# Performance work log

Hardware: AMD Instinct MI355X
Metric: run time of the kernel (lower is better)

Reference implementation:

```python
import jax, jax.numpy as jnp
import numpy as np

N_NODES = 50000
N_EDGES = 800000
IN_DIM = 512
HEADS = 4
HID = 64
OUT = 64
NEG_SLOPE = 0.2  # DGL GATConv default


def gat_layer(x, W, attn_l, attn_r, bias, src, dst, n_nodes, heads, d_out):
    # x: [N, F_in], W: [F_in, heads*d_out], attn_l/attn_r: [heads, d_out], bias: [heads, d_out]
    f = (x @ W).reshape(n_nodes, heads, d_out)          # [N, H, D]
    el = jnp.sum(f * attn_l, axis=-1)                   # [N, H]
    er = jnp.sum(f * attn_r, axis=-1)                   # [N, H]
    e = jax.nn.leaky_relu(el[src] + er[dst], NEG_SLOPE) # [E, H]
    # segment softmax over incoming edges of each dst node
    m = jax.ops.segment_max(e, dst, num_segments=n_nodes)       # [N, H]
    ex = jnp.exp(e - m[dst])                                     # [E, H]
    den = jax.ops.segment_sum(ex, dst, num_segments=n_nodes)    # [N, H]
    a = ex / den[dst]                                            # [E, H]
    # scatter-aggregate weighted messages
    out = jax.ops.segment_sum(a[:, :, None] * f[src], dst, num_segments=n_nodes)  # [N, H, D]
    return out + bias, a


def setup_inputs() -> dict:
    key = jax.random.key(0)
    ks = jax.random.split(key, 12)
    features = jax.random.normal(ks[0], (N_NODES, IN_DIM), dtype=jnp.float32)
    src = jax.random.randint(ks[1], (N_EDGES,), 0, N_NODES, dtype=jnp.int32)
    dst = jax.random.randint(ks[2], (N_EDGES,), 0, N_NODES, dtype=jnp.int32)
    s1 = 1.0 / np.sqrt(IN_DIM)
    s2 = 1.0 / np.sqrt(HEADS * HID)
    W1 = jax.random.normal(ks[3], (IN_DIM, HEADS * HID), dtype=jnp.float32) * s1
    al1 = jax.random.normal(ks[4], (HEADS, HID), dtype=jnp.float32) * s1
    ar1 = jax.random.normal(ks[5], (HEADS, HID), dtype=jnp.float32) * s1
    b1 = jnp.zeros((HEADS, HID), dtype=jnp.float32)
    W2 = jax.random.normal(ks[6], (HEADS * HID, OUT), dtype=jnp.float32) * s2
    al2 = jax.random.normal(ks[7], (1, OUT), dtype=jnp.float32) * s2
    ar2 = jax.random.normal(ks[8], (1, OUT), dtype=jnp.float32) * s2
    b2 = jnp.zeros((1, OUT), dtype=jnp.float32)
    return {"features": features, "W1": W1, "al1": al1, "ar1": ar1, "b1": b1,
            "W2": W2, "al2": al2, "ar2": ar2, "b2": b2, "src": src, "dst": dst}


def reference(features, W1, al1, ar1, b1, W2, al2, ar2, b2, src, dst):
    h1, _ = gat_layer(features, W1, al1, ar1, b1, src, dst, N_NODES, HEADS, HID)
    h1 = jax.nn.elu(h1.reshape(N_NODES, HEADS * HID))   # flatten heads + ELU
    h2, _ = gat_layer(h1, W2, al2, ar2, b2, src, dst, N_NODES, 1, OUT)
    return h2  # [N, 1, OUT]
```

## Files before the change

### kernel.cpp

```cpp
#include <hip/hip_runtime.h>

#define N_NODES 50000
#define N_EDGES 800000
#define IN_DIM 512
#define NEG_SLOPE 0.2f

typedef short short8 __attribute__((ext_vector_type(8)));
typedef float f32x16 __attribute__((ext_vector_type(16)));
typedef __attribute__((address_space(3))) unsigned int lds_u32;
typedef const __attribute__((address_space(1))) unsigned int glb_u32;

__device__ __forceinline__ unsigned bf16rne(float f) {
  union { float f; unsigned u; } v;
  v.f = f;
  return (v.u + 0x7FFFu + ((v.u >> 16) & 1u)) >> 16;
}
__device__ __forceinline__ void tsplit8(float4 a, float4 b, short8& hi,
                                        short8& lo) {
  float fa[8] = {a.x, a.y, a.z, a.w, b.x, b.y, b.z, b.w};
#pragma unroll
  for (int i = 0; i < 8; i++) {
    unsigned u = __float_as_uint(fa[i]);
    hi[i] = (short)(u >> 16);
    float lof = fa[i] - __uint_as_float(u & 0xffff0000u);
    lo[i] = (short)(__float_as_uint(lof) >> 16);
  }
}

__global__ void pack_w(const float* __restrict__ W, short* __restrict__ Bhi,
                       int N) {
  int k = blockIdx.x, n = threadIdx.x;
  float w = W[(size_t)k * N + n];
  int ksub = k >> 4, kh = (k >> 3) & 1, j = k & 7;
  int nsub = n >> 5, lane2 = (n & 31) | (kh << 5);
  size_t off = (((size_t)ksub * (N >> 5) + nsub) * 64 + lane2) * 8 + j;
  Bhi[off] = (short)bf16rne(w);
}

template <int K, int NSUBS, int NTILES>
__global__ __launch_bounds__(256) void gemm_mfma(
    const float* __restrict__ A, const short* __restrict__ Bhi_,
    unsigned short* __restrict__ Cb, const float* __restrict__ alv,
    const float* __restrict__ arv, float* __restrict__ el,
    float* __restrict__ er, int M) {
  constexpr int N = NSUBS * 32;
  constexpr int MT = 4 / NTILES;
  constexpr int BROWS = MT * 32;
  constexpr int T = K / 32;
  __shared__ float ldsb[2][BROWS * 32];

  const int tid = threadIdx.x;
  const int lane = tid & 63;
  const int w = tid >> 6;
  const int l31 = lane & 31;
  const int half = lane >> 5;
  const int local_mt = w / NTILES;
  const int ntile = w % NTILES;
  const int block_row0 = blockIdx.x * BROWS;

  const float* gsrc[MT];
#pragma unroll
  for (int q = 0; q < MT; q++) {
    int seg = w * MT + q;
    int r = seg * 8 + (lane >> 3);
    int c = (lane & 7) ^ (r & 7);
    int grow = block_row0 + r;
    if (grow > M - 1) grow = M - 1;
    gsrc[q] = A + (size_t)grow * K + c * 4;
  }
  unsigned lbase[MT];
#pragma unroll
  for (int q = 0; q < MT; q++) lbase[q] = (w * MT + q) * 256;

  const short8* bh = (const short8*)Bhi_;
  const size_t bbase = (size_t)(ntile * 2) * 64 + lane;

  const int arow = local_mt * 32 + l31;
  const int rs = arow & 7;

  f32x16 acc0 = {}, acc1 = {};
  short8 cb0[2], cb1[2];

#pragma unroll
  for (int q = 0; q < MT; q++) {
    __builtin_amdgcn_global_load_lds((glb_u32*)(gsrc[q]),
                                     (lds_u32*)&ldsb[0][lbase[q]], 16, 0, 0);
  }
#pragma unroll
  for (int u = 0; u < 2; u++) {
    size_t bb = bbase + (size_t)u * NSUBS * 64;
    cb0[u] = bh[bb];
    cb1[u] = bh[bb + 64];
  }
  __syncthreads();

  int buf = 0;
  for (int t = 0; t < T; t++) {
    if (t + 1 < T) {
      int kb = (t + 1) * 32;
#pragma unroll
      for (int q = 0; q < MT; q++) {
        __builtin_amdgcn_global_load_lds((glb_u32*)(gsrc[q] + kb),
                                         (lds_u32*)&ldsb[buf ^ 1][lbase[q]],
                                         16, 0, 0);
      }
    }
    int tn = (t + 1 < T) ? t + 1 : t;
    short8 nb0[2], nb1[2];
#pragma unroll
    for (int u = 0; u < 2; u++) {
      size_t bb = bbase + (size_t)(tn * 2 + u) * NSUBS * 64;
      nb0[u] = bh[bb];
      nb1[u] = bh[bb + 64];
    }
    const float* lb = ldsb[buf];
#pragma unroll
    for (int u = 0; u < 2; u++) {
      int c0 = u * 4 + half * 2;
      float4 a0 = *(const float4*)&lb[arow * 32 + (c0 ^ rs) * 4];
      float4 a1 = *(const float4*)&lb[arow * 32 + ((c0 + 1) ^ rs) * 4];
      short8 ah, al8;
      tsplit8(a0, a1, ah, al8);
      acc0 = __builtin_amdgcn_mfma_f32_32x32x16_bf16(ah, cb0[u], acc0, 0, 0, 0);
      acc0 = __builtin_amdgcn_mfma_f32_32x32x16_bf16(al8, cb0[u], acc0, 0, 0, 0);
      acc1 = __builtin_amdgcn_mfma_f32_32x32x16_bf16(ah, cb1[u], acc1, 0, 0, 0);
      acc1 = __builtin_amdgcn_mfma_f32_32x32x16_bf16(al8, cb1[u], acc1, 0, 0, 0);
    }
    __syncthreads();
#pragma unroll
    for (int u = 0; u < 2; u++) {
      cb0[u] = nb0[u];
      cb1[u] = nb1[u];
    }
    buf ^= 1;
  }

  int colbase = ntile * 64 + l31;
  float wa0 = alv[colbase], wa1 = alv[colbase + 32];
  float wr0 = arv[colbase], wr1 = arv[colbase + 32];
  const int mrow0 = block_row0 + local_mt * 32;
#pragma unroll
  for (int r = 0; r < 16; r++) {
    int roff = (r & 3) + 8 * (r >> 2) + 4 * half;
    int row = mrow0 + roff;
    if (row < M) {
      Cb[(size_t)row * N + colbase] = (unsigned short)bf16rne(acc0[r]);
      Cb[(size_t)row * N + colbase + 32] = (unsigned short)bf16rne(acc1[r]);
    }
    float elv = acc0[r] * wa0 + acc1[r] * wa1;
    float erv = acc0[r] * wr0 + acc1[r] * wr1;
#pragma unroll
    for (int off = 1; off < 32; off <<= 1) {
      elv += __shfl_xor(elv, off);
      erv += __shfl_xor(erv, off);
    }
    if (l31 == 0 && row < M) {
      el[row * NTILES + ntile] = elv;
      er[row * NTILES + ntile] = erv;
    }
  }
}

__global__ void hist_kernel(const int* __restrict__ dst,
                            int* __restrict__ counts) {
  int e = blockIdx.x * blockDim.x + threadIdx.x;
  if (e < N_EDGES) atomicAdd(&counts[dst[e]], 1);
}

#define NSCAN 196
__global__ __launch_bounds__(256) void scan_part(const int* __restrict__ counts,
                                                 int* __restrict__ offsets,
                                                 int* __restrict__ bsums) {
  __shared__ int sh[256];
  int t = threadIdx.x;
  int i = blockIdx.x * 256 + t;
  int v = (i < N_NODES) ? counts[i] : 0;
  sh[t] = v;
  __syncthreads();
  for (int o = 1; o < 256; o <<= 1) {
    int x = (t >= o) ? sh[t - o] : 0;
    __syncthreads();
    sh[t] += x;
    __syncthreads();
  }
  if (i < N_NODES) offsets[i] = sh[t] - v;
  if (t == 255) bsums[blockIdx.x] = sh[255];
}
__global__ __launch_bounds__(256) void scan_top(int* __restrict__ bsums) {
  __shared__ int sh[256];
  int t = threadIdx.x;
  int v = (t < NSCAN) ? bsums[t] : 0;
  sh[t] = v;
  __syncthreads();
  for (int o = 1; o < 256; o <<= 1) {
    int x = (t >= o) ? sh[t - o] : 0;
    __syncthreads();
    sh[t] += x;
    __syncthreads();
  }
  if (t < NSCAN) bsums[t] = sh[t] - v;
}
__global__ __launch_bounds__(256) void scan_add(int* __restrict__ offsets,
                                                const int* __restrict__ bsums) {
  int i = blockIdx.x * 256 + threadIdx.x;
  if (i < N_NODES) offsets[i] += bsums[blockIdx.x];
  if (i == 0) offsets[N_NODES] = N_EDGES;
}

__global__ void scatter_kernel(const int* __restrict__ src,
                               const int* __restrict__ dst,
                               const int* __restrict__ offsets,
                               int* __restrict__ fill,
                               int* __restrict__ csr_src) {
  int e = blockIdx.x * blockDim.x + threadIdx.x;
  if (e < N_EDGES) {
    int d = dst[e];
    int pos = offsets[d] + atomicAdd(&fill[d], 1);
    csr_src[pos] = src[e];
  }
}

__global__ __launch_bounds__(256) void agg1_kernel(
    const int* __restrict__ offsets, const int* __restrict__ csr_src,
    const float* __restrict__ el, const float* __restrict__ er,
    const unsigned short* __restrict__ fb, const float* __restrict__ bias,
    float* __restrict__ h1) {
  __shared__ float red[3][256];
  __shared__ float dred[3][32];
  int n = blockIdx.x;
  int t = threadIdx.x;
  int w = t >> 6, lane = t & 63;
  int l31 = lane & 31;
  int eslot = lane >> 5;
  int h = l31 >> 3;
  int slot = w * 2 + eslot;
  int off0 = offsets[n], deg = offsets[n + 1] - off0;
  float erh = er[n * 4 + h];
  float4 aLo = {0.f, 0.f, 0.f, 0.f}, aHi = {0.f, 0.f, 0.f, 0.f};
  float4 bLo = {0.f, 0.f, 0.f, 0.f}, bHi = {0.f, 0.f, 0.f, 0.f};
  float sden = 0.f;
  int i = slot;
  for (; i + 8 < deg; i += 16) {
    int s0 = csr_src[off0 + i];
    int s1 = csr_src[off0 + i + 8];
    uint4 p0 = *(const uint4*)(fb + (size_t)s0 * 256 + l31 * 8);
    uint4 p1 = *(const uint4*)(fb + (size_t)s1 * 256 + l31 * 8);
    float e0 = el[s0 * 4 + h] + erh;
    float e1 = el[s1 * 4 + h] + erh;
    e0 = e0 > 0.f ? e0 : NEG_SLOPE * e0;
    e1 = e1 > 0.f ? e1 : NEG_SLOPE * e1;
    float a0 = __expf(e0), a1 = __expf(e1);
    sden += a0 + a1;
    aLo.x += a0 * __uint_as_float(p0.x << 16);
    aLo.y += a0 * __uint_as_float(p0.x & 0xffff0000u);
    aLo.z += a0 * __uint_as_float(p0.y << 16);
    aLo.w += a0 * __uint_as_float(p0.y & 0xffff0000u);
    aHi.x += a0 * __uint_as_float(p0.z << 16);
    aHi.y += a0 * __uint_as_float(p0.z & 0xffff0000u);
    aHi.z += a0 * __uint_as_float(p0.w << 16);
    aHi.w += a0 * __uint_as_float(p0.w & 0xffff0000u);
    bLo.x += a1 * __uint_as_float(p1.x << 16);
    bLo.y += a1 * __uint_as_float(p1.x & 0xffff0000u);
    bLo.z += a1 * __uint_as_float(p1.y << 16);
    bLo.w += a1 * __uint_as_float(p1.y & 0xffff0000u);
    bHi.x += a1 * __uint_as_float(p1.z << 16);
    bHi.y += a1 * __uint_as_float(p1.z & 0xffff0000u);
    bHi.z += a1 * __uint_as_float(p1.w << 16);
    bHi.w += a1 * __uint_as_float(p1.w & 0xffff0000u);
  }
  if (i < deg) {
    int s0 = csr_src[off0 + i];
    uint4 p0 = *(const uint4*)(fb + (size_t)s0 * 256 + l31 * 8);
    float e0 = el[s0 * 4 + h] + erh;
    e0 = e0 > 0.f ? e0 : NEG_SLOPE * e0;
    float a0 = __expf(e0);
    sden += a0;
    aLo.x += a0 * __uint_as_float(p0.x << 16);
    aLo.y += a0 * __uint_as_float(p0.x & 0xffff0000u);
    aLo.z += a0 * __uint_as_float(p0.y << 16);
    aLo.w += a0 * __uint_as_float(p0.y & 0xffff0000u);
    aHi.x += a0 * __uint_as_float(p0.z << 16);
    aHi.y += a0 * __uint_as_float(p0.z & 0xffff0000u);
    aHi.z += a0 * __uint_as_float(p0.w << 16);
    aHi.w += a0 * __uint_as_float(p0.w & 0xffff0000u);
  }
  aLo.x += bLo.x; aLo.y += bLo.y; aLo.z += bLo.z; aLo.w += bLo.w;
  aHi.x += bHi.x; aHi.y += bHi.y; aHi.z += bHi.z; aHi.w += bHi.w;
  aLo.x += __shfl_xor(aLo.x, 32);
  aLo.y += __shfl_xor(aLo.y, 32);
  aLo.z += __shfl_xor(aLo.z, 32);
  aLo.w += __shfl_xor(aLo.w, 32);
  aHi.x += __shfl_xor(aHi.x, 32);
  aHi.y += __shfl_xor(aHi.y, 32);
  aHi.z += __shfl_xor(aHi.z, 32);
  aHi.w += __shfl_xor(aHi.w, 32);
  sden += __shfl_xor(sden, 32);
  if (w && lane < 32) {
    *(float4*)(&red[w - 1][l31 * 8]) = aLo;
    *(float4*)(&red[w - 1][l31 * 8 + 4]) = aHi;
    dred[w - 1][l31] = sden;
  }
  __syncthreads();
  if (w == 0 && lane < 32) {
    float den = sden;
#pragma unroll
    for (int j = 0; j < 3; j++) {
      float4 rL = *(float4*)(&red[j][l31 * 8]);
      float4 rH = *(float4*)(&red[j][l31 * 8 + 4]);
      aLo.x += rL.x; aLo.y += rL.y; aLo.z += rL.z; aLo.w += rL.w;
      aHi.x += rH.x; aHi.y += rH.y; aHi.z += rH.z; aHi.w += rH.w;
      den += dred[j][l31];
    }
    float invd = den > 0.f ? 1.0f / den : 0.f;
    float4 b0 = ((const float4*)bias)[l31 * 2];
    float4 b1 = ((const float4*)bias)[l31 * 2 + 1];
    float o[8] = {aLo.x * invd + b0.x, aLo.y * invd + b0.y,
                  aLo.z * invd + b0.z, aLo.w * invd + b0.w,
                  aHi.x * invd + b1.x, aHi.y * invd + b1.y,
                  aHi.z * invd + b1.z, aHi.w * invd + b1.w};
#pragma unroll
    for (int j = 0; j < 8; j++) o[j] = o[j] > 0.f ? o[j] : __expf(o[j]) - 1.0f;
    float4 o0 = {o[0], o[1], o[2], o[3]};
    float4 o1 = {o[4], o[5], o[6], o[7]};
    *(float4*)(h1 + (size_t)n * 256 + l31 * 8) = o0;
    *(float4*)(h1 + (size_t)n * 256 + l31 * 8 + 4) = o1;
  }
}

__global__ __launch_bounds__(256) void agg2_kernel(
    const int* __restrict__ offsets, const int* __restrict__ csr_src,
    const float* __restrict__ el, const float* __restrict__ er,
    const unsigned short* __restrict__ fb2, const float* __restrict__ bias,
    float* __restrict__ out) {
  int w = threadIdx.x >> 6, lane = threadIdx.x & 63;
  int n = blockIdx.x * 4 + w;
  if (n >= N_NODES) return;
  int dg = lane & 15, eslot = lane >> 4;
  int off0 = offsets[n], deg = offsets[n + 1] - off0;
  float ern = er[n];
  float4 acc = {0.f, 0.f, 0.f, 0.f};
  float4 acc2 = {0.f, 0.f, 0.f, 0.f};
  float sden = 0.f;
  int i = eslot;
  for (; i + 4 < deg; i += 8) {
    int s0 = csr_src[off0 + i];
    int s1 = csr_src[off0 + i + 4];
    uint2 p0 = *(const uint2*)(fb2 + (size_t)s0 * 64 + dg * 4);
    uint2 p1 = *(const uint2*)(fb2 + (size_t)s1 * 64 + dg * 4);
    float e0 = el[s0] + ern;
    float e1 = el[s1] + ern;
    e0 = e0 > 0.f ? e0 : NEG_SLOPE * e0;
    e1 = e1 > 0.f ? e1 : NEG_SLOPE * e1;
    float a0 = __expf(e0), a1 = __expf(e1);
    sden += a0 + a1;
    acc.x += a0 * __uint_as_float(p0.x << 16);
    acc.y += a0 * __uint_as_float(p0.x & 0xffff0000u);
    acc.z += a0 * __uint_as_float(p0.y << 16);
    acc.w += a0 * __uint_as_float(p0.y & 0xffff0000u);
    acc2.x += a1 * __uint_as_float(p1.x << 16);
    acc2.y += a1 * __uint_as_float(p1.x & 0xffff0000u);
    acc2.z += a1 * __uint_as_float(p1.y << 16);
    acc2.w += a1 * __uint_as_float(p1.y & 0xffff0000u);
  }
  if (i < deg) {
    int s0 = csr_src[off0 + i];
    uint2 p0 = *(const uint2*)(fb2 + (size_t)s0 * 64 + dg * 4);
    float e0 = el[s0] + ern;
    e0 = e0 > 0.f ? e0 : NEG_SLOPE * e0;
    float a0 = __expf(e0);
    sden += a0;
    acc.x += a0 * __uint_as_float(p0.x << 16);
    acc.y += a0 * __uint_as_float(p0.x & 0xffff0000u);
    acc.z += a0 * __uint_as_float(p0.y << 16);
    acc.w += a0 * __uint_as_float(p0.y & 0xffff0000u);
  }
  acc.x += acc2.x;
  acc.y += acc2.y;
  acc.z += acc2.z;
  acc.w += acc2.w;
#pragma unroll
  for (int off = 16; off < 64; off <<= 1) {
    acc.x += __shfl_xor(acc.x, off);
    acc.y += __shfl_xor(acc.y, off);
    acc.z += __shfl_xor(acc.z, off);
    acc.w += __shfl_xor(acc.w, off);
    sden += __shfl_xor(sden, off);
  }
  if (eslot == 0) {
    float invd = sden > 0.f ? 1.0f / sden : 0.f;
    float4 b = ((const float4*)bias)[dg];
    float4 ov = {acc.x * invd + b.x, acc.y * invd + b.y, acc.z * invd + b.z,
                 acc.w * invd + b.w};
    *(float4*)(out + (size_t)n * 64 + dg * 4) = ov;
  }
}

extern "C" void kernel_launch(void* const* d_in, const int* in_sizes, int n_in,
                              void* d_out, int out_size, void* d_ws,
                              size_t ws_size, hipStream_t stream) {
  const float* features = (const float*)d_in[0];
  const float* W1 = (const float*)d_in[1];
  const float* al1 = (const float*)d_in[2];
  const float* ar1 = (const float*)d_in[3];
  const float* b1 = (const float*)d_in[4];
  const float* W2 = (const float*)d_in[5];
  const float* al2 = (const float*)d_in[6];
  const float* ar2 = (const float*)d_in[7];
  const float* b2 = (const float*)d_in[8];
  const int* src = (const int*)d_in[9];
  const int* dst = (const int*)d_in[10];
  float* out = (float*)d_out;

  float* h1 = (float*)d_ws;
  unsigned short* fb = (unsigned short*)(h1 + (size_t)N_NODES * 256);
  unsigned short* fb2 = fb;
  float* el1 = (float*)(fb + (size_t)N_NODES * 256);
  float* er1 = el1 + N_NODES * 4;
  float* el2 = er1 + N_NODES * 4;
  float* er2 = el2 + N_NODES;
  int* counts = (int*)(er2 + N_NODES);
  int* offsets = counts + N_NODES;
  int* fill = offsets + N_NODES + 1;
  int* csr_src = fill + N_NODES;
  int* bsums = csr_src + N_EDGES;

  short* b1hi = (short*)d_out;
  short* b2hi = (short*)fill;

  hipMemsetAsync(counts, 0, N_NODES * sizeof(int), stream);
  hipMemsetAsync(fill, 0, N_NODES * sizeof(int), stream);
  hist_kernel<<<(N_EDGES + 255) / 256, 256, 0, stream>>>(dst, counts);
  scan_part<<<NSCAN, 256, 0, stream>>>(counts, offsets, bsums);
  scan_top<<<1, 256, 0, stream>>>(bsums);
  scan_add<<<NSCAN, 256, 0, stream>>>(offsets, bsums);
  scatter_kernel<<<(N_EDGES + 255) / 256, 256, 0, stream>>>(src, dst, offsets,
                                                            fill, csr_src);

  pack_w<<<512, 256, 0, stream>>>(W1, b1hi, 256);
  pack_w<<<256, 64, 0, stream>>>(W2, b2hi, 64);

  gemm_mfma<IN_DIM, 8, 4><<<1563, 256, 0, stream>>>(features, b1hi, fb, al1,
                                                    ar1, el1, er1, N_NODES);
  agg1_kernel<<<N_NODES, 256, 0, stream>>>(offsets, csr_src, el1, er1, fb, b1,
                                           h1);

  gemm_mfma<256, 2, 1><<<391, 256, 0, stream>>>(h1, b2hi, fb2, al2, ar2, el2,
                                                er2, N_NODES);
  agg2_kernel<<<(N_NODES + 3) / 4, 256, 0, stream>>>(offsets, csr_src, el2,
                                                     er2, fb2, b2, out);
}
```

Measured before the change: 408.2 us.

## Deepen GEMM K-step to 64 and add row-group register blocking

The MFMA GEMM now stages 64-wide K slices per iteration instead of 32, halving the number of barrier-separated steps, and adds an RG template parameter so each wave computes multiple 32-row groups, reusing loaded B fragments across them. Layer 1 uses RG=2, which halves the grid, and launch bounds request two blocks per CU. This is meant to cut per-step sync overhead and B-fragment loads, in exchange for more LDS and register use, which may lower occupancy.

```diff
diff --git a/kernel.cpp b/kernel.cpp
--- a/kernel.cpp
+++ b/kernel.cpp
@@ -37,17 +37,18 @@
   Bhi[off] = (short)bf16rne(w);
 }
 
-template <int K, int NSUBS, int NTILES>
-__global__ __launch_bounds__(256) void gemm_mfma(
+template <int K, int NSUBS, int NTILES, int RG>
+__global__ __launch_bounds__(256, 2) void gemm_mfma(
     const float* __restrict__ A, const short* __restrict__ Bhi_,
     unsigned short* __restrict__ Cb, const float* __restrict__ alv,
     const float* __restrict__ arv, float* __restrict__ el,
     float* __restrict__ er, int M) {
   constexpr int N = NSUBS * 32;
   constexpr int MT = 4 / NTILES;
-  constexpr int BROWS = MT * 32;
-  constexpr int T = K / 32;
-  __shared__ float ldsb[2][BROWS * 32];
+  constexpr int BROWS = MT * RG * 32;
+  constexpr int T = K / 64;
+  constexpr int GPW = BROWS / 16;
+  __shared__ float ldsb[2][BROWS * 64];
 
   const int tid = threadIdx.x;
   const int lane = tid & 63;
@@ -58,79 +59,89 @@
   const int ntile = w % NTILES;
   const int block_row0 = blockIdx.x * BROWS;
 
-  const float* gsrc[MT];
-#pragma unroll
-  for (int q = 0; q < MT; q++) {
-    int seg = w * MT + q;
-    int r = seg * 8 + (lane >> 3);
-    int c = (lane & 7) ^ (r & 7);
+  const float* gsrc[GPW];
+#pragma unroll
+  for (int q = 0; q < GPW; q++) {
+    int g = w * GPW + q;
+    int r = g * 4 + (lane >> 4);
+    int p = lane & 15;
+    int c = (p & 8) | ((p & 7) ^ (r & 7));
     int grow = block_row0 + r;
     if (grow > M - 1) grow = M - 1;
     gsrc[q] = A + (size_t)grow * K + c * 4;
   }
-  unsigned lbase[MT];
-#pragma unroll
-  for (int q = 0; q < MT; q++) lbase[q] = (w * MT + q) * 256;
 
   const short8* bh = (const short8*)Bhi_;
-  const size_t bbase = (size_t)(ntile * 2) * 64 + lane;
-
-  const int arow = local_mt * 32 + l31;
-  const int rs = arow & 7;
-
-  f32x16 acc0 = {}, acc1 = {};
-  short8 cb0[2], cb1[2];
-
-#pragma unroll
-  for (int q = 0; q < MT; q++) {
-    __builtin_amdgcn_global_load_lds((glb_u32*)(gsrc[q]),
-                                     (lds_u32*)&ldsb[0][lbase[q]], 16, 0, 0);
-  }
-#pragma unroll
-  for (int u = 0; u < 2; u++) {
-    size_t bb = bbase + (size_t)u * NSUBS * 64;
-    cb0[u] = bh[bb];
-    cb1[u] = bh[bb + 64];
+
+  f32x16 acc[RG][2] = {};
+  short8 cb[4][2], nb[4][2];
+
+#pragma unroll
+  for (int q = 0; q < GPW; q++) {
+    __builtin_amdgcn_global_load_lds(
+        (glb_u32*)(gsrc[q]), (lds_u32*)&ldsb[0][(w * GPW + q) * 256], 16, 0,
+        0);
+  }
+#pragma unroll
+  for (int s = 0; s < 4; s++) {
+#pragma unroll
+    for (int g = 0; g < 2; g++) {
+      cb[s][g] = bh[(size_t)(s * NSUBS + ntile * 2 + g) * 64 + lane];
+    }
   }
   __syncthreads();
 
   int buf = 0;
   for (int t = 0; t < T; t++) {
     if (t + 1 < T) {
-      int kb = (t + 1) * 32;
-#pragma unroll
-      for (int q = 0; q < MT; q++) {
-        __builtin_amdgcn_global_load_lds((glb_u32*)(gsrc[q] + kb),
-                                         (lds_u32*)&ldsb[buf ^ 1][lbase[q]],
-                                         16, 0, 0);
-      }
-    }
-    int tn = (t + 1 < T) ? t + 1 : t;
-    short8 nb0[2], nb1[2];
-#pragma unroll
-    for (int u = 0; u < 2; u++) {
-      size_t bb = bbase + (size_t)(tn * 2 + u) * NSUBS * 64;
-      nb0[u] = bh[bb];
-      nb1[u] = bh[bb + 64];
+      int kb = (t + 1) * 64;
+#pragma unroll
+      for (int q = 0; q < GPW; q++) {
+        __builtin_amdgcn_global_load_lds(
+            (glb_u32*)(gsrc[q] + kb),
+            (lds_u32*)&ldsb[buf ^ 1][(w * GPW + q) * 256], 16, 0, 0);
+      }
+#pragma unroll
+      for (int s = 0; s < 4; s++) {
+#pragma unroll
+        for (int g = 0; g < 2; g++) {
+          nb[s][g] =
+              bh[(size_t)(((t + 1) * 4 + s) * NSUBS + ntile * 2 + g) * 64 +
+                 lane];
+        }
+      }
     }
     const float* lb = ldsb[buf];
 #pragma unroll
-    for (int u = 0; u < 2; u++) {
-      int c0 = u * 4 + half * 2;
-      float4 a0 = *(const float4*)&lb[arow * 32 + (c0 ^ rs) * 4];
-      float4 a1 = *(const float4*)&lb[arow * 32 + ((c0 + 1) ^ rs) * 4];
-      short8 ah, al8;
-      tsplit8(a0, a1, ah, al8);
-      acc0 = __builtin_amdgcn_mfma_f32_32x32x16_bf16(ah, cb0[u], acc0, 0, 0, 0);
-      acc0 = __builtin_amdgcn_mfma_f32_32x32x16_bf16(al8, cb0[u], acc0, 0, 0, 0);
-      acc1 = __builtin_amdgcn_mfma_f32_32x32x16_bf16(ah, cb1[u], acc1, 0, 0, 0);
-      acc1 = __builtin_amdgcn_mfma_f32_32x32x16_bf16(al8, cb1[u], acc1, 0, 0, 0);
+    for (int rg = 0; rg < RG; rg++) {
+      const int arow = local_mt * RG * 32 + rg * 32 + l31;
+      const int rs = arow & 7;
+#pragma unroll
+      for (int s = 0; s < 4; s++) {
+        int c0 = s * 4 + half * 2;
+        int p0 = (c0 & 8) | ((c0 & 7) ^ rs);
+        int p1 = ((c0 + 1) & 8) | (((c0 + 1) & 7) ^ rs);
+        float4 a0 = *(const float4*)&lb[arow * 64 + p0 * 4];
+        float4 a1 = *(const float4*)&lb[arow * 64 + p1 * 4];
+        short8 ah, al8;
+        tsplit8(a0, a1, ah, al8);
+        acc[rg][0] =
+            __builtin_amdgcn_mfma_f32_32x32x16_bf16(ah, cb[s][0], acc[rg][0], 0, 0, 0);
+        acc[rg][0] =
+            __builtin_amdgcn_mfma_f32_32x32x16_bf16(al8, cb[s][0], acc[rg][0], 0, 0, 0);
+        acc[rg][1] =
+            __builtin_amdgcn_mfma_f32_32x32x16_bf16(ah, cb[s][1], acc[rg][1], 0, 0, 0);
+        acc[rg][1] =
+            __builtin_amdgcn_mfma_f32_32x32x16_bf16(al8, cb[s][1], acc[rg][1], 0, 0, 0);
+      }
     }
     __syncthreads();
-#pragma unroll
-    for (int u = 0; u < 2; u++) {
-      cb0[u] = nb0[u];
-      cb1[u] = nb1[u];
+    if (t + 1 < T) {
+#pragma unroll
+      for (int s = 0; s < 4; s++) {
+#pragma unroll
+        for (int g = 0; g < 2; g++) cb[s][g] = nb[s][g];
+      }
     }
     buf ^= 1;
   }
@@ -138,25 +149,29 @@
   int colbase = ntile * 64 + l31;
   float wa0 = alv[colbase], wa1 = alv[colbase + 32];
   float wr0 = arv[colbase], wr1 = arv[colbase + 32];
-  const int mrow0 = block_row0 + local_mt * 32;
-#pragma unroll
-  for (int r = 0; r < 16; r++) {
-    int roff = (r & 3) + 8 * (r >> 2) + 4 * half;
-    int row = mrow0 + roff;
-    if (row < M) {
-      Cb[(size_t)row * N + colbase] = (unsigned short)bf16rne(acc0[r]);
-      Cb[(size_t)row * N + colbase + 32] = (unsigned short)bf16rne(acc1[r]);
-    }
-    float elv = acc0[r] * wa0 + acc1[r] * wa1;
-    float erv = acc0[r] * wr0 + acc1[r] * wr1;
-#pragma unroll
-    for (int off = 1; off < 32; off <<= 1) {
-      elv += __shfl_xor(elv, off);
-      erv += __shfl_xor(erv, off);
-    }
-    if (l31 == 0 && row < M) {
-      el[row * NTILES + ntile] = elv;
-      er[row * NTILES + ntile] = erv;
+#pragma unroll
+  for (int rg = 0; rg < RG; rg++) {
+    const int mrow0 = block_row0 + local_mt * RG * 32 + rg * 32;
+#pragma unroll
+    for (int r = 0; r < 16; r++) {
+      int roff = (r & 3) + 8 * (r >> 2) + 4 * half;
+      int row = mrow0 + roff;
+      if (row < M) {
+        Cb[(size_t)row * N + colbase] = (unsigned short)bf16rne(acc[rg][0][r]);
+        Cb[(size_t)row * N + colbase + 32] =
+            (unsigned short)bf16rne(acc[rg][1][r]);
+      }
+      float elv = acc[rg][0][r] * wa0 + acc[rg][1][r] * wa1;
+      float erv = acc[rg][0][r] * wr0 + acc[rg][1][r] * wr1;
+#pragma unroll
+      for (int off = 1; off < 32; off <<= 1) {
+        elv += __shfl_xor(elv, off);
+        erv += __shfl_xor(erv, off);
+      }
+      if (l31 == 0 && row < M) {
+        el[row * NTILES + ntile] = elv;
+        er[row * NTILES + ntile] = erv;
+      }
     }
   }
 }
@@ -439,13 +454,13 @@
   pack_w<<<512, 256, 0, stream>>>(W1, b1hi, 256);
   pack_w<<<256, 64, 0, stream>>>(W2, b2hi, 64);
 
-  gemm_mfma<IN_DIM, 8, 4><<<1563, 256, 0, stream>>>(features, b1hi, fb, al1,
-                                                    ar1, el1, er1, N_NODES);
+  gemm_mfma<IN_DIM, 8, 4, 2><<<782, 256, 0, stream>>>(features, b1hi, fb, al1,
+                                                      ar1, el1, er1, N_NODES);
   agg1_kernel<<<N_NODES, 256, 0, stream>>>(offsets, csr_src, el1, er1, fb, b1,
                                            h1);
 
-  gemm_mfma<256, 2, 1><<<391, 256, 0, stream>>>(h1, b2hi, fb2, al2, ar2, el2,
-                                                er2, N_NODES);
+  gemm_mfma<256, 2, 1, 1><<<391, 256, 0, stream>>>(h1, b2hi, fb2, al2, ar2,
+                                                   el2, er2, N_NODES);
   agg2_kernel<<<(N_NODES + 3) / 4, 256, 0, stream>>>(offsets, csr_src, el2,
                                                      er2, fb2, b2, out);
 }
```

Measured after the change: 407.8 us. No clear change (-0.1%).

## Stage B tiles through LDS with async loads and explicit vmcnt waits

Applied to the files above, without the earlier changes.

The GEMM main loop now copies the pre-packed bf16 B tiles into double-buffered LDS with global_load_lds, alongside the A tiles, instead of having each wave load B straight into registers. It replaces __syncthreads with explicit s_waitcnt vmcnt(5) plus raw barriers, so the next stage's loads stay in flight while the current stage is computed. This is meant to share B loads across waves and overlap memory with MFMA work. It hardcodes the count of outstanding loads per wave, enforced by a static_assert, and uses more LDS per block, which may lower occupancy.

```diff
diff --git a/kernel.cpp b/kernel.cpp
--- a/kernel.cpp
+++ b/kernel.cpp
@@ -47,7 +47,11 @@
   constexpr int MT = 4 / NTILES;
   constexpr int BROWS = MT * 32;
   constexpr int T = K / 32;
-  __shared__ float ldsb[2][BROWS * 32];
+  constexpr int GB = NSUBS / 2;
+  constexpr int BSTEP_S = NSUBS * 1024;
+  static_assert(MT + GB == 5, "vmcnt literals assume 5 loads/wave/step");
+  __shared__ float ldsA[2][BROWS * 32];
+  __shared__ short ldsB[2][BSTEP_S];
 
   const int tid = threadIdx.x;
   const int lane = tid & 63;
@@ -58,7 +62,7 @@
   const int ntile = w % NTILES;
   const int block_row0 = blockIdx.x * BROWS;
 
-  const float* gsrc[MT];
+  const float* gsrcA[MT];
 #pragma unroll
   for (int q = 0; q < MT; q++) {
     int seg = w * MT + q;
@@ -66,72 +70,61 @@
     int c = (lane & 7) ^ (r & 7);
     int grow = block_row0 + r;
     if (grow > M - 1) grow = M - 1;
-    gsrc[q] = A + (size_t)grow * K + c * 4;
-  }
-  unsigned lbase[MT];
-#pragma unroll
-  for (int q = 0; q < MT; q++) lbase[q] = (w * MT + q) * 256;
-
-  const short8* bh = (const short8*)Bhi_;
-  const size_t bbase = (size_t)(ntile * 2) * 64 + lane;
+    gsrcA[q] = A + (size_t)grow * K + c * 4;
+  }
+  const short* bsrc = Bhi_ + lane * 8;
 
   const int arow = local_mt * 32 + l31;
   const int rs = arow & 7;
 
   f32x16 acc0 = {}, acc1 = {};
-  short8 cb0[2], cb1[2];
-
-#pragma unroll
-  for (int q = 0; q < MT; q++) {
-    __builtin_amdgcn_global_load_lds((glb_u32*)(gsrc[q]),
-                                     (lds_u32*)&ldsb[0][lbase[q]], 16, 0, 0);
-  }
-#pragma unroll
-  for (int u = 0; u < 2; u++) {
-    size_t bb = bbase + (size_t)u * NSUBS * 64;
-    cb0[u] = bh[bb];
-    cb1[u] = bh[bb + 64];
-  }
-  __syncthreads();
+
+  auto STAGE = [&](int b, int t) {
+#pragma unroll
+    for (int q = 0; q < MT; q++) {
+      __builtin_amdgcn_global_load_lds((glb_u32*)(gsrcA[q] + t * 32),
+                                       (lds_u32*)&ldsA[b][(w * MT + q) * 256],
+                                       16, 0, 0);
+    }
+#pragma unroll
+    for (int j = 0; j < GB; j++) {
+      __builtin_amdgcn_global_load_lds(
+          (glb_u32*)(bsrc + (size_t)t * BSTEP_S + (w * GB + j) * 512),
+          (lds_u32*)&ldsB[b][(w * GB + j) * 512], 16, 0, 0);
+    }
+  };
+
+  STAGE(0, 0);
 
   int buf = 0;
   for (int t = 0; t < T; t++) {
     if (t + 1 < T) {
-      int kb = (t + 1) * 32;
-#pragma unroll
-      for (int q = 0; q < MT; q++) {
-        __builtin_amdgcn_global_load_lds((glb_u32*)(gsrc[q] + kb),
-                                         (lds_u32*)&ldsb[buf ^ 1][lbase[q]],
-                                         16, 0, 0);
-      }
-    }
-    int tn = (t + 1 < T) ? t + 1 : t;
-    short8 nb0[2], nb1[2];
+      STAGE(buf ^ 1, t + 1);
+      asm volatile("s_waitcnt vmcnt(5)" ::: "memory");
+    } else {
+      asm volatile("s_waitcnt vmcnt(0)" ::: "memory");
+    }
+    __builtin_amdgcn_s_barrier();
+
+    const float* lA = ldsA[buf];
+    const short* lB = ldsB[buf];
 #pragma unroll
     for (int u = 0; u < 2; u++) {
-      size_t bb = bbase + (size_t)(tn * 2 + u) * NSUBS * 64;
-      nb0[u] = bh[bb];
-      nb1[u] = bh[bb + 64];
-    }
-    const float* lb = ldsb[buf];
-#pragma unroll
-    for (int u = 0; u < 2; u++) {
+      short8 cb0 = *(const short8*)&lB[(u * NSUBS + ntile * 2) * 512 + lane * 8];
+      short8 cb1 =
+          *(const short8*)&lB[(u * NSUBS + ntile * 2 + 1) * 512 + lane * 8];
       int c0 = u * 4 + half * 2;
-      float4 a0 = *(const float4*)&lb[arow * 32 + (c0 ^ rs) * 4];
-      float4 a1 = *(const float4*)&lb[arow * 32 + ((c0 + 1) ^ rs) * 4];
+      float4 a0 = *(const float4*)&lA[arow * 32 + (c0 ^ rs) * 4];
+      float4 a1 = *(const float4*)&lA[arow * 32 + ((c0 + 1) ^ rs) * 4];
       short8 ah, al8;
       tsplit8(a0, a1, ah, al8);
-      acc0 = __builtin_amdgcn_mfma_f32_32x32x16_bf16(ah, cb0[u], acc0, 0, 0, 0);
-      acc0 = __builtin_amdgcn_mfma_f32_32x32x16_bf16(al8, cb0[u], acc0, 0, 0, 0);
-      acc1 = __builtin_amdgcn_mfma_f32_32x32x16_bf16(ah, cb1[u], acc1, 0, 0, 0);
-      acc1 = __builtin_amdgcn_mfma_f32_32x32x16_bf16(al8, cb1[u], acc1, 0, 0, 0);
-    }
-    __syncthreads();
-#pragma unroll
-    for (int u = 0; u < 2; u++) {
-      cb0[u] = nb0[u];
-      cb1[u] = nb1[u];
-    }
+      acc0 = __builtin_amdgcn_mfma_f32_32x32x16_bf16(ah, cb0, acc0, 0, 0, 0);
+      acc0 = __builtin_amdgcn_mfma_f32_32x32x16_bf16(al8, cb0, acc0, 0, 0, 0);
+      acc1 = __builtin_amdgcn_mfma_f32_32x32x16_bf16(ah, cb1, acc1, 0, 0, 0);
+      acc1 = __builtin_amdgcn_mfma_f32_32x32x16_bf16(al8, cb1, acc1, 0, 0, 0);
+    }
+    asm volatile("s_waitcnt lgkmcnt(0)" ::: "memory");
+    __builtin_amdgcn_s_barrier();
     buf ^= 1;
   }
 
```

New measurement: 404.8 us. Within noise of the previous version (-0.8%).
